# Kernel tuning notes

Hardware: AMD Instinct MI355X
Metric: run time of the kernel (lower is better)

## Reference

```python
import jax, jax.numpy as jnp
import numpy as np

NUM_METAPATHS = 3
ETYPES = np.array([[0, 1], [2, 3], [4, 5]])  # [P, L-1], indices into expanded r_vec
N_NODES = 100000
N_TARGETS = 8192
E = 250000
L = 3
IN_DIM = 64
NUM_HEADS = 8
ATTN_VEC_DIM = 128
OUT_DIM = 64
ALPHA = 0.01  # LeakyReLU slope


def setup_inputs() -> dict:
    key = jax.random.key(0)
    ks = jax.random.split(key, 10)
    features = jax.random.normal(ks[0], (N_NODES, IN_DIM), jnp.float32)
    indices = jax.random.randint(ks[1], (NUM_METAPATHS, E, L), 0, N_NODES)
    dst = jax.random.randint(ks[2], (NUM_METAPATHS, E), 0, N_TARGETS)
    r_vec = jax.random.normal(ks[3], (3, IN_DIM // 2, 2), jnp.float32) * 0.5
    attn = jax.random.normal(ks[4], (NUM_METAPATHS, NUM_HEADS, IN_DIM), jnp.float32) * 0.1
    fc1_w = jax.random.normal(ks[5], (ATTN_VEC_DIM, IN_DIM * NUM_HEADS), jnp.float32) * 0.05
    fc1_b = jnp.zeros((ATTN_VEC_DIM,), jnp.float32)
    fc2_w = jax.random.normal(ks[6], (1, ATTN_VEC_DIM), jnp.float32) * 0.1
    fc_w = jax.random.normal(ks[7], (OUT_DIM, IN_DIM * NUM_HEADS), jnp.float32) * 0.05
    fc_b = jnp.zeros((OUT_DIM,), jnp.float32)
    return dict(features=features, indices=indices, dst=dst, r_vec=r_vec, attn=attn,
                fc1_w=fc1_w, fc1_b=fc1_b, fc2_w=fc2_w, fc_w=fc_w, fc_b=fc_b)


def _cmul(a, b):
    # complex multiply on trailing [..., 2] (real, imag) pairs
    re = a[..., 0] * b[..., 0] - a[..., 1] * b[..., 1]
    im = a[..., 0] * b[..., 1] + a[..., 1] * b[..., 0]
    return jnp.stack([re, im], axis=-1)


def _final_r_vec(r_full):
    # r_full: [num_edge_type, d2, 2] -> cumulative rotations per metapath [P, L, d2, 2]
    d2 = r_full.shape[1]
    one = jnp.stack([jnp.ones((d2,), r_full.dtype), jnp.zeros((d2,), r_full.dtype)], axis=-1)
    finals = []
    for p in range(NUM_METAPATHS):
        f = [None] * L
        f[L - 1] = one
        for i in range(L - 2, -1, -1):
            f[i] = _cmul(f[i + 1], r_full[int(ETYPES[p, i])])
        finals.append(jnp.stack(f))
    return jnp.stack(finals)  # [P, L, d2, 2]


def _forward(features, indices, dst, r_vec, attn, fc1_w, fc1_b, fc2_w, fc_w, fc_b):
    d2 = IN_DIM // 2
    # RotatE0: L2-normalize each complex rotation, then expand with conjugates
    r = r_vec / jnp.sqrt(jnp.sum(r_vec * r_vec, axis=-1, keepdims=True))
    r_conj = r * jnp.array([1.0, -1.0], r.dtype)
    r_full = jnp.stack([r, r_conj], axis=1).reshape(-1, d2, 2)  # [num_edge_type, d2, 2]
    final_r = _final_r_vec(r_full)  # [P, L, d2, 2]; final[L-1] = 1+0j (identity)

    def per_metapath(idx, d_idx, final_rv, attn_p):
        # idx: [E, L] node ids, d_idx: [E] destination (target) ids
        edata = features[idx].reshape(E, L, d2, 2)           # gather metapath instances
        edata = _cmul(edata, final_rv[None])                 # rotate each position
        hidden = edata.reshape(E, L, IN_DIM).mean(axis=1)    # [E, d]
        eft = jnp.broadcast_to(hidden[:, None, :], (E, NUM_HEADS, IN_DIM))
        a = jnp.einsum('ehd,hd->eh', eft, attn_p)
        a = jnp.where(a > 0, a, ALPHA * a)                   # leaky_relu
        # edge softmax per destination segment (stable)
        a_max = jax.ops.segment_max(a, d_idx, num_segments=N_TARGETS)
        a = jnp.exp(a - a_max[d_idx])
        a_sum = jax.ops.segment_sum(a, d_idx, num_segments=N_TARGETS)
        a = a / a_sum[d_idx]
        ft = jax.ops.segment_sum(eft * a[:, :, None], d_idx, num_segments=N_TARGETS)
        return ft.reshape(N_TARGETS, NUM_HEADS * IN_DIM)

    outs = jax.vmap(per_metapath)(indices, dst, final_r, attn)  # [P, Nt, H*d]
    outs = jax.nn.elu(outs)
    # inter-metapath attention
    fc1 = jnp.tanh(jnp.einsum('pnd,ad->pna', outs, fc1_w) + fc1_b)  # [P, Nt, A]
    beta = fc1.mean(axis=1) @ fc2_w.T                               # [P, 1]
    beta = jax.nn.softmax(beta[:, 0])                               # [P]
    h = jnp.einsum('p,pnd->nd', beta, outs)                         # [Nt, H*d]
    h_fc = h @ fc_w.T + fc_b                                        # [Nt, out_dim]
    return h_fc, h


def reference(features, indices, dst, r_vec, attn, fc1_w, fc1_b, fc2_w, fc_w, fc_b):
    return _forward(features, indices, dst, r_vec, attn, fc1_w, fc1_b, fc2_w, fc_w, fc_b)
```

## Files before the change

kernel.cpp:

```cpp
#include <hip/hip_runtime.h>
#include <hip/hip_bf16.h>
#include <hip/hip_fp16.h>

#define NP   3
#define NE   250000
#define NL   3
#define NT   8192
#define NN   100000
#define IND  64
#define ND2  32
#define NH   8
#define NAD  128
#define NOD  64
#define NHD  512
#define LALPHA 0.01f
#define NSEG (NP*NT)
#define NB   16

typedef __attribute__((ext_vector_type(8))) _Float16 half8;
typedef __attribute__((ext_vector_type(4))) _Float16 half4;
typedef __attribute__((ext_vector_type(4))) float f32x4;

#define FLAG_W    0
#define FINALR_W  64
#define ATILDE_W  704
#define BETAACC_N 5376
#define BETA_N    5760
#define COUNTS_N  6144
#define OFFS_N    30720
#define CURSOR_N  55360
#define EIDX_N    80000
#define ATTNF_N   3080000
#define FC1W_N    3081600
#define FC1B_N    3147136
#define FC2W_N    3147264
#define FCW_N     3147392
#define FCB_N     3180160
#define RVEC_N    3180224
#define FEATH_N   3180544
#define SCORE_N   6380544
#define OUTS_N    13580544
#define NEED_WORDS 19872000UL

#define BETAACC_F 1024
#define BETA_F    1472
#define COUNTS_F  2048
#define OFFS_F    26624
#define CURSOR_F  51264
#define ELIST_F   75904
#define FEATF_F   825920
#define ATTNF_F   7225920
#define FC1W_F    7227456
#define FC1B_F    7292992
#define FC2W_F    7293120
#define FCW_F     7293248
#define FCB_F     7326016
#define RVEC_F    7326080
#define OUTS_F    7326272

__device__ __forceinline__ float bf2f(unsigned short u) {
    union { unsigned int i; float f; } c; c.i = ((unsigned int)u) << 16; return c.f;
}

__global__ __launch_bounds__(256) void k_prep(
        const unsigned short* __restrict__ feat_raw,
        const void* __restrict__ rvec_src, const void* __restrict__ attn_src,
        const void* __restrict__ fc1b_src, const void* __restrict__ fc2w_src,
        const void* __restrict__ fcb_src,
        float* __restrict__ ws, int* __restrict__ flag,
        int* __restrict__ counts, float* __restrict__ betaacc,
        float* __restrict__ rvecf, float* __restrict__ attnf,
        float* __restrict__ fc1bf, float* __restrict__ fc2wf,
        float* __restrict__ fcbf) {
    __shared__ int cnt;
    int t = threadIdx.x;
    if (t == 0) cnt = 0;
    __syncthreads();
    int wild = 0;
    for (int i = t; i < 512; i += 256) {
        unsigned short u = feat_raw[i];
        int e = (u >> 7) & 0xFF;
        if (u != 0 && (e < 0x60 || e > 0x90)) wild++;
    }
    for (int off = 32; off; off >>= 1) wild += __shfl_xor(wild, off);
    if ((t & 63) == 0) atomicAdd(&cnt, wild);
    __syncthreads();
    int f = cnt > 64 ? 1 : 0;
    if (t == 0) *flag = f;
    for (int i = t; i < NSEG; i += 256) counts[i] = 0;
    for (int i = t; i < NP * NAD; i += 256) betaacc[i] = 0.f;
    for (int i = t; i < 192; i += 256)
        rvecf[i] = f ? ((const float*)rvec_src)[i] : bf2f(((const unsigned short*)rvec_src)[i]);
    for (int i = t; i < 1536; i += 256)
        attnf[i] = f ? ((const float*)attn_src)[i] : bf2f(((const unsigned short*)attn_src)[i]);
    if (t < 128) fc1bf[t] = f ? ((const float*)fc1b_src)[t] : bf2f(((const unsigned short*)fc1b_src)[t]);
    if (t < 128) fc2wf[t] = f ? ((const float*)fc2w_src)[t] : bf2f(((const unsigned short*)fc2w_src)[t]);
    if (t < 64)  fcbf[t]  = f ? ((const float*)fcb_src)[t]  : bf2f(((const unsigned short*)fcb_src)[t]);
    __syncthreads();
    if (t < NP * ND2) {
        int p = t / ND2, j = t % ND2;
        float re = rvecf[(p * ND2 + j) * 2 + 0];
        float im = rvecf[(p * ND2 + j) * 2 + 1];
        float inv = rsqrtf(re * re + im * im);
        float nre = re * inv, nim = im * inv;
        float f1r = nre, f1i = -nim;
        float f0r = f1r * nre - f1i * nim;
        float f0i = f1r * nim + f1i * nre;
        float* fr = ws + FINALR_W + p * NL * ND2 * 2;
        fr[(0 * ND2 + j) * 2 + 0] = f0r; fr[(0 * ND2 + j) * 2 + 1] = f0i;
        fr[(1 * ND2 + j) * 2 + 0] = f1r; fr[(1 * ND2 + j) * 2 + 1] = f1i;
        fr[(2 * ND2 + j) * 2 + 0] = 1.f; fr[(2 * ND2 + j) * 2 + 1] = 0.f;
    }
    __syncthreads();
    const float* finalr = ws + FINALR_W;
    float* atil = ws + ATILDE_W;
    for (int i = t; i < NP * NL * NH * IND; i += 256) {
        int d = i & 63, h = (i >> 6) & 7, l = (i >> 9) % 3, p = i / (64 * 8 * 3);
        int j = d >> 1; bool im = (d & 1) != 0;
        float cr = finalr[(p * NL * ND2 + l * ND2 + j) * 2 + 0];
        float ci = finalr[(p * NL * ND2 + l * ND2 + j) * 2 + 1];
        float ar = attnf[(p * NH + h) * IND + 2 * j];
        float ai = attnf[(p * NH + h) * IND + 2 * j + 1];
        float v = im ? (ai * cr - ar * ci) : (ar * cr + ai * ci);
        atil[i] = v * (1.f / 3.f);
    }
}

__global__ void k_cvt(const void* __restrict__ src, float* __restrict__ dst, int n,
                      const int* __restrict__ flag) {
    int i = blockIdx.x * blockDim.x + threadIdx.x;
    if (i >= n) return;
    if (*flag) dst[i] = ((const float*)src)[i];
    else       dst[i] = bf2f(((const unsigned short*)src)[i]);
}

__global__ void k_cvt_h4(const void* __restrict__ src, half4* __restrict__ dst, int n4,
                         const int* __restrict__ flag) {
    int i = blockIdx.x * blockDim.x + threadIdx.x;
    if (i >= n4) return;
    half4 o;
    if (*flag) {
        float4 v = ((const float4*)src)[i];
        o[0] = (_Float16)v.x; o[1] = (_Float16)v.y; o[2] = (_Float16)v.z; o[3] = (_Float16)v.w;
    } else {
        ushort4 u = ((const ushort4*)src)[i];
        o[0] = (_Float16)bf2f(u.x); o[1] = (_Float16)bf2f(u.y);
        o[2] = (_Float16)bf2f(u.z); o[3] = (_Float16)bf2f(u.w);
    }
    dst[i] = o;
}

__global__ void k_cvt_tr(const void* __restrict__ src, float* __restrict__ dst,
                         int R, int C, const int* __restrict__ flag) {
    int i = blockIdx.x * blockDim.x + threadIdx.x;
    if (i >= R * C) return;
    int r = i / C, c = i % C;
    float v;
    if (*flag) v = ((const float*)src)[i];
    else       v = bf2f(((const unsigned short*)src)[i]);
    dst[c * R + r] = v;
}

__global__ __launch_bounds__(256) void k_score(const _Float16* __restrict__ feat,
                                               const float* __restrict__ atil,
                                               float* __restrict__ S) {
    __shared__ float xs[128][68];
    __shared__ float as[72][68];
    int t = threadIdx.x;
    int nbase = blockIdx.x * 128;
    for (int i = t; i < 72 * 64; i += 256) as[i >> 6][i & 63] = atil[i];
    for (int i = t; i < 128 * 8; i += 256) {
        int node = nbase + (i >> 3), seg = i & 7;
        if (node < NN) {
            half8 v = *(const half8*)(feat + (long)node * IND + seg * 8);
#pragma unroll
            for (int j = 0; j < 8; j++) xs[i >> 3][seg * 8 + j] = (float)v[j];
        } else {
#pragma unroll
            for (int j = 0; j < 8; j++) xs[i >> 3][seg * 8 + j] = 0.f;
        }
    }
    __syncthreads();
    int lane = t & 63, w = t >> 6;
    int g = lane >> 3, h = lane & 7;
    int nloc = (w * 8 + g) * 4;
    float acc[9][4];
#pragma unroll
    for (int c = 0; c < 9; c++)
#pragma unroll
        for (int u = 0; u < 4; u++) acc[c][u] = 0.f;
    for (int ch = 0; ch < 16; ch++) {
        float4 xv[4];
#pragma unroll
        for (int u = 0; u < 4; u++) xv[u] = *(const float4*)&xs[nloc + u][ch * 4];
#pragma unroll
        for (int c = 0; c < 9; c++) {
            float4 av = *(const float4*)&as[c * 8 + h][ch * 4];
#pragma unroll
            for (int u = 0; u < 4; u++)
                acc[c][u] += xv[u].x * av.x + xv[u].y * av.y + xv[u].z * av.z + xv[u].w * av.w;
        }
    }
#pragma unroll
    for (int u = 0; u < 4; u++) {
        int node = nbase + nloc + u;
        if (node < NN) {
#pragma unroll
            for (int c = 0; c < 9; c++)
                S[(long)node * 72 + c * 8 + h] = acc[c][u];
        }
    }
}

__global__ void k_count(const int* __restrict__ dst, int* __restrict__ counts) {
    int id = blockIdx.x * blockDim.x + threadIdx.x;
    if (id >= NP * NE) return;
    int p = id / NE;
    atomicAdd(&counts[p * NT + dst[id]], 1);
}

__global__ __launch_bounds__(256) void k_scan(const int* __restrict__ counts,
                                              int* __restrict__ offs,
                                              int* __restrict__ cursor) {
    __shared__ int wtot[4];
    int t = threadIdx.x;
    const int CH = NSEG / 256;
    int base = t * CH;
    int s = 0;
    for (int i = 0; i < CH; i++) s += counts[base + i];
    int l = t & 63, w = t >> 6;
    int v = s;
    for (int off = 1; off < 64; off <<= 1) {
        int u = __shfl_up(v, off);
        if (l >= off) v += u;
    }
    if (l == 63) wtot[w] = v;
    __syncthreads();
    int wb = 0;
    for (int i = 0; i < w; i++) wb += wtot[i];
    int run = wb + v - s;
    for (int i = 0; i < CH; i++) {
        int c = counts[base + i];
        offs[base + i] = run; cursor[base + i] = run;
        run += c;
    }
    if (t == 255) offs[NSEG] = wb + v;
}

__global__ void k_scatter2(const int* __restrict__ dst, const int* __restrict__ indices,
                           int* __restrict__ cursor, int4* __restrict__ eidx) {
    int id = blockIdx.x * blockDim.x + threadIdx.x;
    if (id >= NP * NE) return;
    int p = id / NE, e = id % NE;
    int pos = atomicAdd(&cursor[p * NT + dst[id]], 1);
    const int* ip = indices + (long)p * NE * NL + (long)e * NL;
    eidx[pos] = make_int4(ip[0], ip[1], ip[2], 0);
}

__global__ void k_scatter(const int* __restrict__ dst, int* __restrict__ cursor,
                          int* __restrict__ elist) {
    int id = blockIdx.x * blockDim.x + threadIdx.x;
    if (id >= NP * NE) return;
    int p = id / NE, e = id % NE;
    int pos = atomicAdd(&cursor[p * NT + dst[id]], 1);
    elist[pos] = e;
}

__global__ __launch_bounds__(64) void k_agg2(
        const _Float16* __restrict__ featH, const int4* __restrict__ eidx,
        const float* __restrict__ S, const float* __restrict__ finalr,
        const int* __restrict__ offs, _Float16* __restrict__ outs) {
    int b = blockIdx.x;
    int p = b / NT;
    int t = threadIdx.x;
    int h = t >> 3, q = t & 7;

    float a0[8], a1[8], a2[8];
#pragma unroll
    for (int r = 0; r < 8; r++) { a0[r] = 0.f; a1[r] = 0.f; a2[r] = 0.f; }
    float se = 0.f;

    int beg = offs[b], end = offs[b + 1];
    const float* Sp = S + p * 24 + h;

    int i = beg;
    for (; i + 4 <= end; i += 4) {
        int4 ee[4];
        float s0v[4], s1v[4], s2v[4];
        half8 x0[4], x1[4], x2[4];
#pragma unroll
        for (int u = 0; u < 4; u++) ee[u] = eidx[i + u];
#pragma unroll
        for (int u = 0; u < 4; u++) {
            s0v[u] = Sp[(long)ee[u].x * 72];
            s1v[u] = Sp[(long)ee[u].y * 72 + 8];
            s2v[u] = Sp[(long)ee[u].z * 72 + 16];
            x0[u] = *(const half8*)(featH + ((long)ee[u].x << 6) + (q << 3));
            x1[u] = *(const half8*)(featH + ((long)ee[u].y << 6) + (q << 3));
            x2[u] = *(const half8*)(featH + ((long)ee[u].z << 6) + (q << 3));
        }
#pragma unroll
        for (int u = 0; u < 4; u++) {
            float s = s0v[u] + s1v[u] + s2v[u];
            float a = s > 0.f ? s : LALPHA * s;
            float eh = __expf(a);
            se += eh;
#pragma unroll
            for (int r = 0; r < 8; r++) {
                a0[r] += eh * (float)x0[u][r];
                a1[r] += eh * (float)x1[u][r];
                a2[r] += eh * (float)x2[u][r];
            }
        }
    }
    for (; i < end; i++) {
        int4 e = eidx[i];
        float s = Sp[(long)e.x * 72] + Sp[(long)e.y * 72 + 8] + Sp[(long)e.z * 72 + 16];
        float a = s > 0.f ? s : LALPHA * s;
        float eh = __expf(a);
        se += eh;
        half8 x0 = *(const half8*)(featH + ((long)e.x << 6) + (q << 3));
        half8 x1 = *(const half8*)(featH + ((long)e.y << 6) + (q << 3));
        half8 x2 = *(const half8*)(featH + ((long)e.z << 6) + (q << 3));
#pragma unroll
        for (int r = 0; r < 8; r++) {
            a0[r] += eh * (float)x0[r];
            a1[r] += eh * (float)x1[r];
            a2[r] += eh * (float)x2[r];
        }
    }

    const float* fr = finalr + p * NL * ND2 * 2;
    float sc = (end > beg) ? (1.f / 3.f) / se : 0.f;
    half8 o;
#pragma unroll
    for (int jj = 0; jj < 4; jj++) {
        int j = 4 * q + jj;
        float c0r = fr[(0 * ND2 + j) * 2 + 0], c0i = fr[(0 * ND2 + j) * 2 + 1];
        float c1r = fr[(1 * ND2 + j) * 2 + 0], c1i = fr[(1 * ND2 + j) * 2 + 1];
        float ar, ai, vr, vi;
        ar = a0[2 * jj]; ai = a0[2 * jj + 1];
        vr = ar * c0r - ai * c0i; vi = ar * c0i + ai * c0r;
        ar = a1[2 * jj]; ai = a1[2 * jj + 1];
        vr += ar * c1r - ai * c1i; vi += ar * c1i + ai * c1r;
        vr += a2[2 * jj]; vi += a2[2 * jj + 1];
        vr *= sc; vi *= sc;
        vr = vr > 0.f ? vr : __expf(vr) - 1.f;
        vi = vi > 0.f ? vi : __expf(vi) - 1.f;
        o[2 * jj]     = (_Float16)vr;
        o[2 * jj + 1] = (_Float16)vi;
    }
    *(half8*)(outs + (long)b * NHD + (h << 6) + (q << 3)) = o;
}

__global__ __launch_bounds__(64) void k_agg(
        const float* __restrict__ feat, const int* __restrict__ indices,
        const float* __restrict__ attn, const float* __restrict__ ws_f,
        const int* __restrict__ offs, const int* __restrict__ elist,
        _Float16* __restrict__ outs) {
    int b = blockIdx.x;
    int p = b / NT;
    int d = threadIdx.x;
    int j = d >> 1;
    bool isim = (d & 1) != 0;
    const float* fr = ws_f + FINALR_W + p * NL * ND2 * 2;
    float cr[NL], ci[NL];
#pragma unroll
    for (int l = 0; l < NL; l++) {
        cr[l] = fr[(l * ND2 + j) * 2 + 0];
        ci[l] = fr[(l * ND2 + j) * 2 + 1];
    }
    float at[NH];
#pragma unroll
    for (int h = 0; h < NH; h++) at[h] = attn[(p * NH + h) * IND + d];
    float ft[NH], se[NH];
#pragma unroll
    for (int h = 0; h < NH; h++) { ft[h] = 0.f; se[h] = 0.f; }
    int beg = offs[b], end = offs[b + 1];
    const int* idxp = indices + (long)p * NE * NL;
    for (int i = beg; i < end; i++) {
        int e = elist[i];
        int nn[3] = { idxp[e * 3 + 0], idxp[e * 3 + 1], idxp[e * 3 + 2] };
        float hid = 0.f;
#pragma unroll
        for (int l = 0; l < NL; l++) {
            float x = feat[(long)nn[l] * IND + d];
            float xp = __shfl_xor(x, 1);
            float re = isim ? xp : x;
            float im = isim ? x : xp;
            hid += isim ? (re * ci[l] + im * cr[l]) : (re * cr[l] - im * ci[l]);
        }
        hid *= (1.f / 3.f);
#pragma unroll
        for (int h = 0; h < NH; h++) {
            float v = hid * at[h];
#pragma unroll
            for (int off = 32; off; off >>= 1) v += __shfl_xor(v, off);
            float a = v > 0.f ? v : LALPHA * v;
            float eh = __expf(a);
            se[h] += eh;
            ft[h] += eh * hid;
        }
    }
    _Float16* orow = outs + (long)b * NHD;
    bool has = end > beg;
#pragma unroll
    for (int h = 0; h < NH; h++) {
        float v = has ? ft[h] / fmaxf(se[h], 1e-20f) : 0.f;
        v = v > 0.f ? v : (__expf(v) - 1.f);
        orow[h * IND + d] = (_Float16)v;
    }
}

__global__ __launch_bounds__(256) void k_fc1(
        const _Float16* __restrict__ outs, const _Float16* __restrict__ fc1h,
        const float* __restrict__ fc1_b, float* __restrict__ betaacc) {
    __shared__ float red[4][NAD];
    int tid = threadIdx.x;
    int wid = tid >> 6, lane = tid & 63;
    int nt = blockIdx.x * 4 + wid;
    int p  = blockIdx.x / (NT / 16 / 4);
    int col = lane & 15, kq = lane >> 4;

    const _Float16* brow  = outs + ((long)nt * 16 + col) * NHD + kq * 8;
    const _Float16* abase = fc1h + (long)col * NHD + kq * 8;

    f32x4 acc[8];
#pragma unroll
    for (int ta = 0; ta < 8; ta++) acc[ta] = (f32x4){0.f, 0.f, 0.f, 0.f};

    for (int kk = 0; kk < 16; kk++) {
        half8 b = *(const half8*)(brow + kk * 32);
#pragma unroll
        for (int ta = 0; ta < 8; ta++) {
            half8 a = *(const half8*)(abase + (long)ta * 16 * NHD + kk * 32);
            acc[ta] = __builtin_amdgcn_mfma_f32_16x16x32_f16(a, b, acc[ta], 0, 0, 0);
        }
    }

#pragma unroll
    for (int ta = 0; ta < 8; ta++) {
#pragma unroll
        for (int r = 0; r < 4; r++) {
            int arow = ta * 16 + kq * 4 + r;
            float v = tanhf(acc[ta][r] + fc1_b[arow]);
            v += __shfl_xor(v, 1); v += __shfl_xor(v, 2);
            v += __shfl_xor(v, 4); v += __shfl_xor(v, 8);
            if (col == 0) red[wid][arow] = v;
        }
    }
    __syncthreads();
    if (tid < NAD) {
        float s = red[0][tid] + red[1][tid] + red[2][tid] + red[3][tid];
        atomicAdd(&betaacc[p * NAD + tid], s);
    }
}

__global__ void k_beta(const float* __restrict__ betaacc,
                       const float* __restrict__ fc2_w, float* __restrict__ beta) {
    __shared__ float lds[NP][NAD];
    int t = threadIdx.x;
    for (int p = 0; p < NP; p++)
        lds[p][t] = betaacc[p * NAD + t] * (1.f / NT) * fc2_w[t];
    __syncthreads();
    if (t == 0) {
        float s[NP];
        for (int p = 0; p < NP; p++) {
            s[p] = 0.f;
            for (int a = 0; a < NAD; a++) s[p] += lds[p][a];
        }
        float m = fmaxf(s[0], fmaxf(s[1], s[2]));
        float e0 = expf(s[0] - m), e1 = expf(s[1] - m), e2 = expf(s[2] - m);
        float inv = 1.f / (e0 + e1 + e2);
        beta[0] = e0 * inv; beta[1] = e1 * inv; beta[2] = e2 * inv;
    }
}

__global__ __launch_bounds__(256) void k_final(
        const _Float16* __restrict__ outs, const float* __restrict__ beta,
        const float* __restrict__ fc_wT, const float* __restrict__ fc_b,
        void* __restrict__ outp, const int* __restrict__ flag) {
    __shared__ float h[NB * NHD];
    __shared__ float part[4 * NB * NOD];
    int n0 = blockIdx.x * NB;
    int t = threadIdx.x;
    int f = *flag;
    float b0 = beta[0], b1 = beta[1], b2 = beta[2];
    const _Float16* o0 = outs + (long)n0 * NHD;
    for (int i = t; i < NB * NHD / 8; i += 256) {
        half8 v0 = *(const half8*)(o0 + i * 8);
        half8 v1 = *(const half8*)(o0 + (long)NT * NHD + i * 8);
        half8 v2 = *(const half8*)(o0 + 2L * NT * NHD + i * 8);
#pragma unroll
        for (int jj = 0; jj < 8; jj++) {
            float v = b0 * (float)v0[jj] + b1 * (float)v1[jj] + b2 * (float)v2[jj];
            h[i * 8 + jj] = v;
            long idx = (long)NT * NOD + (long)n0 * NHD + i * 8 + jj;
            if (f) ((float*)outp)[idx] = v;
            else   ((__hip_bfloat16*)outp)[idx] = __float2bfloat16(v);
        }
    }
    __syncthreads();
    int w = t >> 6, l = t & 63;
    float acc[NB];
#pragma unroll
    for (int n = 0; n < NB; n++) acc[n] = 0.f;
    for (int k = w * 128; k < (w + 1) * 128; k++) {
        float wv = fc_wT[k * NOD + l];
#pragma unroll
        for (int n = 0; n < NB; n++) acc[n] += h[n * NHD + k] * wv;
    }
#pragma unroll
    for (int n = 0; n < NB; n++) part[(w * NB + n) * NOD + l] = acc[n];
    __syncthreads();
    for (int idx = t; idx < NB * NOD; idx += 256) {
        int n = idx >> 6, ll = idx & 63;
        float v = part[(0 * NB + n) * NOD + ll] + part[(1 * NB + n) * NOD + ll]
                + part[(2 * NB + n) * NOD + ll] + part[(3 * NB + n) * NOD + ll]
                + fc_b[ll];
        long oidx = (long)(n0 + n) * NOD + ll;
        if (f) ((float*)outp)[oidx] = v;
        else   ((__hip_bfloat16*)outp)[oidx] = __float2bfloat16(v);
    }
}

extern "C" void kernel_launch(void* const* d_in, const int* in_sizes, int n_in,
                              void* d_out, int out_size, void* d_ws, size_t ws_size,
                              hipStream_t stream) {
    const int* indices = (const int*)d_in[1];
    const int* dst     = (const int*)d_in[2];

    float* ws  = (float*)d_ws;
    int*   wsi = (int*)d_ws;

    bool big = ws_size >= NEED_WORDS * 4UL;

    const int betaacc = big ? BETAACC_N : BETAACC_F;
    const int beta    = big ? BETA_N    : BETA_F;
    const int counts  = big ? COUNTS_N  : COUNTS_F;
    const int offs    = big ? OFFS_N    : OFFS_F;
    const int cursor  = big ? CURSOR_N  : CURSOR_F;
    const int attnf   = big ? ATTNF_N   : ATTNF_F;
    const int fc1w    = big ? FC1W_N    : FC1W_F;
    const int fc1b    = big ? FC1B_N    : FC1B_F;
    const int fc2w    = big ? FC2W_N    : FC2W_F;
    const int fcw     = big ? FCW_N     : FCW_F;
    const int fcb     = big ? FCB_N     : FCB_F;
    const int rvec    = big ? RVEC_N    : RVEC_F;
    const int outsw   = big ? OUTS_N    : OUTS_F;
    _Float16* outsp = (_Float16*)(ws + outsw);
    _Float16* fc1h  = (_Float16*)(ws + fc1w);

    k_prep<<<1, 256, 0, stream>>>((const unsigned short*)d_in[0],
                                  d_in[3], d_in[4], d_in[6], d_in[7], d_in[9],
                                  ws, wsi + FLAG_W, wsi + counts, ws + betaacc,
                                  ws + rvec, ws + attnf, ws + fc1b, ws + fc2w,
                                  ws + fcb);

    k_cvt_h4<<<(NAD * NHD / 4 + 255) / 256, 256, 0, stream>>>(d_in[5], (half4*)fc1h,
                                                              NAD * NHD / 4, wsi + FLAG_W);
    k_cvt_tr<<<(NOD * NHD + 255) / 256, 256, 0, stream>>>(d_in[8], ws + fcw,
                                                          NOD, NHD, wsi + FLAG_W);
    k_count<<<(NP * NE + 255) / 256, 256, 0, stream>>>(dst, wsi + counts);
    k_scan<<<1, 256, 0, stream>>>(wsi + counts, wsi + offs, wsi + cursor);

    if (big) {
        _Float16* featH = (_Float16*)(ws + FEATH_N);
        k_cvt_h4<<<(NN * IND / 4 + 255) / 256, 256, 0, stream>>>(d_in[0], (half4*)featH,
                                                                 NN * IND / 4, wsi + FLAG_W);
        k_score<<<(NN + 127) / 128, 256, 0, stream>>>(featH, ws + ATILDE_W, ws + SCORE_N);
        k_scatter2<<<(NP * NE + 255) / 256, 256, 0, stream>>>(dst, indices,
                                                              wsi + cursor,
                                                              (int4*)(wsi + EIDX_N));
        k_agg2<<<NSEG, 64, 0, stream>>>(featH, (const int4*)(wsi + EIDX_N),
                                        ws + SCORE_N, ws + FINALR_W,
                                        wsi + offs, outsp);
    } else {
        k_cvt<<<(NN * IND + 255) / 256, 256, 0, stream>>>(d_in[0], ws + FEATF_F,
                                                          NN * IND, wsi + FLAG_W);
        k_scatter<<<(NP * NE + 255) / 256, 256, 0, stream>>>(dst, wsi + cursor,
                                                             wsi + ELIST_F);
        k_agg<<<NSEG, 64, 0, stream>>>(ws + FEATF_F, indices, ws + attnf, ws,
                                       wsi + offs, wsi + ELIST_F, outsp);
    }

    k_fc1<<<NP * NT / 16 / 4, 256, 0, stream>>>(outsp, fc1h, ws + fc1b, ws + betaacc);
    k_beta<<<1, 128, 0, stream>>>(ws + betaacc, ws + fc2w, ws + beta);
    k_final<<<NT / NB, 256, 0, stream>>>(outsp, ws + beta, ws + fcw, ws + fcb,
                                         d_out, wsi + FLAG_W);
}
```

Before: 340.6 us.

## Fuse feature fp16 conversion into score kernel, memset counters, 32-bit gather offsets

Drops the separate feature-to-fp16 conversion kernel: the score kernel now reads the raw features, converts them to float for its own use, and writes the fp16 copy that aggregation later reads. Counter and beta-accumulator zeroing moves out of the single-block prep kernel into hipMemsetAsync calls. The aggregation kernel computes gather addresses with 32-bit unsigned byte offsets to cut 64-bit address arithmetic. This saves one kernel launch and one full pass over the feature array, at the cost of two extra memset operations on the stream.

```diff
diff --git a/kernel.cpp b/kernel.cpp
--- a/kernel.cpp
+++ b/kernel.cpp
@@ -68,7 +68,6 @@
         const void* __restrict__ fc1b_src, const void* __restrict__ fc2w_src,
         const void* __restrict__ fcb_src,
         float* __restrict__ ws, int* __restrict__ flag,
-        int* __restrict__ counts, float* __restrict__ betaacc,
         float* __restrict__ rvecf, float* __restrict__ attnf,
         float* __restrict__ fc1bf, float* __restrict__ fc2wf,
         float* __restrict__ fcbf) {
@@ -87,8 +86,6 @@
     __syncthreads();
     int f = cnt > 64 ? 1 : 0;
     if (t == 0) *flag = f;
-    for (int i = t; i < NSEG; i += 256) counts[i] = 0;
-    for (int i = t; i < NP * NAD; i += 256) betaacc[i] = 0.f;
     for (int i = t; i < 192; i += 256)
         rvecf[i] = f ? ((const float*)rvec_src)[i] : bf2f(((const unsigned short*)rvec_src)[i]);
     for (int i = t; i < 1536; i += 256)
@@ -161,23 +158,36 @@
     dst[c * R + r] = v;
 }
 
-__global__ __launch_bounds__(256) void k_score(const _Float16* __restrict__ feat,
+__global__ __launch_bounds__(256) void k_score(const void* __restrict__ feat_src,
+                                               const int* __restrict__ flag,
                                                const float* __restrict__ atil,
-                                               float* __restrict__ S) {
+                                               float* __restrict__ S,
+                                               _Float16* __restrict__ featH) {
     __shared__ float xs[128][68];
     __shared__ float as[72][68];
     int t = threadIdx.x;
     int nbase = blockIdx.x * 128;
+    int f = *flag;
     for (int i = t; i < 72 * 64; i += 256) as[i >> 6][i & 63] = atil[i];
-    for (int i = t; i < 128 * 8; i += 256) {
-        int node = nbase + (i >> 3), seg = i & 7;
+    for (int c = t; c < 2048; c += 256) {
+        int nloc = c >> 4, cc = c & 15;
+        int node = nbase + nloc;
+        float4 v;
         if (node < NN) {
-            half8 v = *(const half8*)(feat + (long)node * IND + seg * 8);
-#pragma unroll
-            for (int j = 0; j < 8; j++) xs[i >> 3][seg * 8 + j] = (float)v[j];
-        } else {
-#pragma unroll
-            for (int j = 0; j < 8; j++) xs[i >> 3][seg * 8 + j] = 0.f;
+            if (f) v = ((const float4*)feat_src)[(size_t)node * 16 + cc];
+            else {
+                ushort4 u = ((const ushort4*)feat_src)[(size_t)node * 16 + cc];
+                v = make_float4(bf2f(u.x), bf2f(u.y), bf2f(u.z), bf2f(u.w));
+            }
+        } else v = make_float4(0.f, 0.f, 0.f, 0.f);
+        int d0 = cc * 4;
+        xs[nloc][d0 + 0] = v.x; xs[nloc][d0 + 1] = v.y;
+        xs[nloc][d0 + 2] = v.z; xs[nloc][d0 + 3] = v.w;
+        if (node < NN) {
+            half4 hv;
+            hv[0] = (_Float16)v.x; hv[1] = (_Float16)v.y;
+            hv[2] = (_Float16)v.z; hv[3] = (_Float16)v.w;
+            *(half4*)(featH + (size_t)node * IND + d0) = hv;
         }
     }
     __syncthreads();
@@ -275,13 +285,17 @@
     int t = threadIdx.x;
     int h = t >> 3, q = t & 7;
 
+    const unsigned sB = (unsigned)((p * 24 + h) * 4);
+    const unsigned fB = (unsigned)(q << 4);
+    const char* Sb = (const char*)S;
+    const char* Fb = (const char*)featH;
+
     float a0[8], a1[8], a2[8];
 #pragma unroll
     for (int r = 0; r < 8; r++) { a0[r] = 0.f; a1[r] = 0.f; a2[r] = 0.f; }
     float se = 0.f;
 
     int beg = offs[b], end = offs[b + 1];
-    const float* Sp = S + p * 24 + h;
 
     int i = beg;
     for (; i + 4 <= end; i += 4) {
@@ -292,12 +306,13 @@
         for (int u = 0; u < 4; u++) ee[u] = eidx[i + u];
 #pragma unroll
         for (int u = 0; u < 4; u++) {
-            s0v[u] = Sp[(long)ee[u].x * 72];
-            s1v[u] = Sp[(long)ee[u].y * 72 + 8];
-            s2v[u] = Sp[(long)ee[u].z * 72 + 16];
-            x0[u] = *(const half8*)(featH + ((long)ee[u].x << 6) + (q << 3));
-            x1[u] = *(const half8*)(featH + ((long)ee[u].y << 6) + (q << 3));
-            x2[u] = *(const half8*)(featH + ((long)ee[u].z << 6) + (q << 3));
+            unsigned ox = (unsigned)ee[u].x, oy = (unsigned)ee[u].y, oz = (unsigned)ee[u].z;
+            s0v[u] = *(const float*)(Sb + (ox * 288u + sB));
+            s1v[u] = *(const float*)(Sb + (oy * 288u + sB) + 32);
+            s2v[u] = *(const float*)(Sb + (oz * 288u + sB) + 64);
+            x0[u] = *(const half8*)(Fb + ((ox << 7) + fB));
+            x1[u] = *(const half8*)(Fb + ((oy << 7) + fB));
+            x2[u] = *(const half8*)(Fb + ((oz << 7) + fB));
         }
 #pragma unroll
         for (int u = 0; u < 4; u++) {
@@ -315,13 +330,16 @@
     }
     for (; i < end; i++) {
         int4 e = eidx[i];
-        float s = Sp[(long)e.x * 72] + Sp[(long)e.y * 72 + 8] + Sp[(long)e.z * 72 + 16];
+        unsigned ox = (unsigned)e.x, oy = (unsigned)e.y, oz = (unsigned)e.z;
+        float s = *(const float*)(Sb + (ox * 288u + sB))
+                + *(const float*)(Sb + (oy * 288u + sB) + 32)
+                + *(const float*)(Sb + (oz * 288u + sB) + 64);
         float a = s > 0.f ? s : LALPHA * s;
         float eh = __expf(a);
         se += eh;
-        half8 x0 = *(const half8*)(featH + ((long)e.x << 6) + (q << 3));
-        half8 x1 = *(const half8*)(featH + ((long)e.y << 6) + (q << 3));
-        half8 x2 = *(const half8*)(featH + ((long)e.z << 6) + (q << 3));
+        half8 x0 = *(const half8*)(Fb + ((ox << 7) + fB));
+        half8 x1 = *(const half8*)(Fb + ((oy << 7) + fB));
+        half8 x2 = *(const half8*)(Fb + ((oz << 7) + fB));
 #pragma unroll
         for (int r = 0; r < 8; r++) {
             a0[r] += eh * (float)x0[r];
@@ -551,9 +569,12 @@
     _Float16* outsp = (_Float16*)(ws + outsw);
     _Float16* fc1h  = (_Float16*)(ws + fc1w);
 
+    hipMemsetAsync((char*)d_ws + (size_t)counts * 4, 0, NSEG * 4, stream);
+    hipMemsetAsync((char*)d_ws + (size_t)betaacc * 4, 0, NP * NAD * 4, stream);
+
     k_prep<<<1, 256, 0, stream>>>((const unsigned short*)d_in[0],
                                   d_in[3], d_in[4], d_in[6], d_in[7], d_in[9],
-                                  ws, wsi + FLAG_W, wsi + counts, ws + betaacc,
+                                  ws, wsi + FLAG_W,
                                   ws + rvec, ws + attnf, ws + fc1b, ws + fc2w,
                                   ws + fcb);
 
@@ -566,9 +587,8 @@
 
     if (big) {
         _Float16* featH = (_Float16*)(ws + FEATH_N);
-        k_cvt_h4<<<(NN * IND / 4 + 255) / 256, 256, 0, stream>>>(d_in[0], (half4*)featH,
-                                                                 NN * IND / 4, wsi + FLAG_W);
-        k_score<<<(NN + 127) / 128, 256, 0, stream>>>(featH, ws + ATILDE_W, ws + SCORE_N);
+        k_score<<<(NN + 127) / 128, 256, 0, stream>>>(d_in[0], wsi + FLAG_W,
+                                                      ws + ATILDE_W, ws + SCORE_N, featH);
         k_scatter2<<<(NP * NE + 255) / 256, 256, 0, stream>>>(dst, indices,
                                                               wsi + cursor,
                                                               (int4*)(wsi + EIDX_N));
```

Result: slower. 354.5 us (+4.1%).
